# Kernel optimization log

Hardware: AMD Instinct MI355X
Metric: run time of the kernel (lower is better)

## Reference

```python
import jax, jax.numpy as jnp
import numpy as np

LOG_2PI = float(np.log(2.0 * np.pi))


def setup_inputs() -> dict:
    key = jax.random.key(0)
    k1, k2, k3 = jax.random.split(key, 3)
    B, C, D = 256, 1000, 256
    return {
        "x": jax.random.normal(k1, (B, D), dtype=jnp.float32),
        "metric_tensor": jax.random.normal(k2, (B, D, D), dtype=jnp.float32),
        "log_priors": jnp.zeros((C,), dtype=jnp.float32),
        "class_means": jax.random.normal(k3, (C, D), dtype=jnp.float32),
        "class_log_vars": jnp.zeros((C, D), dtype=jnp.float32),
    }


def reference(x, metric_tensor, log_priors, class_means, class_log_vars):
    D = x.shape[-1]
    # diff: [B, C, D]
    diff = x[:, None, :] - class_means[None, :, :]
    # Mahalanobis quadratic form per (batch, class): diff^T G diff
    maha = jnp.einsum("bcd,bde,bce->bc", diff, metric_tensor, diff)
    log_likelihood = -0.5 * (maha + jnp.sum(class_log_vars, axis=-1)[None, :] + D * LOG_2PI)
    log_posteriors = log_likelihood + log_priors[None, :]
    return jax.nn.log_softmax(log_posteriors, axis=-1)
```

## Files before the change

### kernel.cpp

```cpp
#include <hip/hip_runtime.h>

#define LOG2PI 1.83787706640934548356f

typedef __attribute__((ext_vector_type(4))) float f32x4;
typedef __attribute__((ext_vector_type(8))) short bf16x8;
typedef __attribute__((ext_vector_type(2))) unsigned int u32x2;

__device__ __forceinline__ unsigned short f2bf(float f) {
    union { float f; unsigned u; } v; v.f = f;
    unsigned r = v.u + 0x7fffu + ((v.u >> 16) & 1u);
    return (unsigned short)(r >> 16);
}
__device__ __forceinline__ bf16x8 pack8(f32x4 a, f32x4 b) {
    bf16x8 h;
    h[0]=(short)f2bf(a[0]); h[1]=(short)f2bf(a[1]); h[2]=(short)f2bf(a[2]); h[3]=(short)f2bf(a[3]);
    h[4]=(short)f2bf(b[0]); h[5]=(short)f2bf(b[1]); h[6]=(short)f2bf(b[2]); h[7]=(short)f2bf(b[3]);
    return h;
}

__global__ __launch_bounds__(256)
void k_prep(const float* __restrict__ clv, const float* __restrict__ lp,
            float* __restrict__ bias)
{
    const int w = threadIdx.x >> 6, lane = threadIdx.x & 63;
    const int c = blockIdx.x * 4 + w;
    if (c >= 1000) return;
    f32x4 v = *reinterpret_cast<const f32x4*>(clv + c * 256 + lane * 4);
    float s = v[0] + v[1] + v[2] + v[3];
    #pragma unroll
    for (int m = 1; m < 64; m <<= 1) s += __shfl_xor(s, m);
    if (lane == 0) bias[c] = lp[c] - 0.5f * (s + 256.0f * LOG2PI);
}

__global__ __launch_bounds__(256, 2)
void k_main(const float* __restrict__ x, const float* __restrict__ G,
            const float* __restrict__ means, float* __restrict__ out)
{
    __shared__ char dbuf[2][8192];
    __shared__ float maha[256];

    const int b     = blockIdx.x >> 2;
    const int cg    = blockIdx.x & 3;
    const int cbase = cg * 256;
    const int tid   = threadIdx.x;
    const int lane  = tid & 63;
    const int wn    = tid >> 6;
    const int lrow  = lane & 15;
    const int g     = lane >> 4;

    const float* Gb = G + (size_t)b * 65536;
    const float* xb = x + b * 256;

    maha[tid] = 0.f;

    bf16x8 greg[4][8];
    #pragma unroll
    for (int n = 0; n < 4; ++n) {
        const float* rowp = Gb + (size_t)(wn * 64 + n * 16 + lrow) * 256 + g * 8;
        #pragma unroll
        for (int ks = 0; ks < 8; ++ks) {
            f32x4 v0 = *reinterpret_cast<const f32x4*>(rowp + ks * 32);
            f32x4 v1 = *reinterpret_cast<const f32x4*>(rowp + ks * 32 + 4);
            greg[n][ks] = pack8(v0, v1);
        }
    }

    const int sr = tid & 15;
    const int s0 = tid >> 4;
    const int e0 = s0 * 8, e1 = e0 + 128;
    const f32x4 xa0 = *reinterpret_cast<const f32x4*>(xb + e0);
    const f32x4 xa1 = *reinterpret_cast<const f32x4*>(xb + e0 + 4);
    const f32x4 xb0 = *reinterpret_cast<const f32x4*>(xb + e1);
    const f32x4 xb1 = *reinterpret_cast<const f32x4*>(xb + e1 + 4);
    const int wbyte0 = (s0 * 16 + (sr ^ ((s0 & 3) << 1))) * 16;
    const int wbyte1 = wbyte0 + 4096;

    f32x4 r0a, r0b, r1a, r1b;
    auto load_chunk = [&](int c0) {
        int cc = cbase + c0 + sr; if (cc > 999) cc = 999;
        const float* mp = means + (size_t)cc * 256;
        r0a = *reinterpret_cast<const f32x4*>(mp + e0);
        r0b = *reinterpret_cast<const f32x4*>(mp + e0 + 4);
        r1a = *reinterpret_cast<const f32x4*>(mp + e1);
        r1b = *reinterpret_cast<const f32x4*>(mp + e1 + 4);
    };
    auto write_chunk = [&](int bufi) {
        *reinterpret_cast<bf16x8*>(dbuf[bufi] + wbyte0) = pack8(xa0 - r0a, xa1 - r0b);
        *reinterpret_cast<bf16x8*>(dbuf[bufi] + wbyte1) = pack8(xb0 - r1a, xb1 - r1b);
    };

    load_chunk(0);

    for (int t = 0; t < 16; ++t) {
        write_chunk(t & 1);
        __syncthreads();
        if (t < 15) load_chunk((t + 1) * 16);

        const char* buf = dbuf[t & 1];
        f32x4 acc[4];
        #pragma unroll
        for (int n = 0; n < 4; ++n) acc[n] = f32x4{0.f, 0.f, 0.f, 0.f};

        #pragma unroll
        for (int ks = 0; ks < 8; ++ks) {
            bf16x8 bfr = *reinterpret_cast<const bf16x8*>(
                buf + ((4 * ks + g) * 16 + (lrow ^ (g << 1))) * 16);
            #pragma unroll
            for (int n = 0; n < 4; ++n)
                acc[n] = __builtin_amdgcn_mfma_f32_16x16x32_bf16(greg[n][ks], bfr, acc[n], 0, 0, 0);
        }

        float p = 0.f;
        #pragma unroll
        for (int n = 0; n < 4; ++n) {
            const int d  = wn * 64 + n * 16 + g * 4;
            const int se = d >> 3;
            const int byte = (se * 16 + (lrow ^ ((se & 3) << 1))) * 16 + (d & 7) * 2;
            u32x2 dv = *reinterpret_cast<const u32x2*>(buf + byte);
            const float f0 = __uint_as_float(dv[0] << 16);
            const float f1 = __uint_as_float(dv[0] & 0xffff0000u);
            const float f2 = __uint_as_float(dv[1] << 16);
            const float f3 = __uint_as_float(dv[1] & 0xffff0000u);
            p += acc[n][0] * f0 + acc[n][1] * f1 + acc[n][2] * f2 + acc[n][3] * f3;
        }
        p += __shfl_xor(p, 16);
        p += __shfl_xor(p, 32);
        if (lane < 16) atomicAdd(&maha[t * 16 + lrow], p);
    }

    __syncthreads();
    const int c = cbase + tid;
    if (c < 1000) out[(size_t)b * 1000 + c] = maha[tid];
}

__global__ __launch_bounds__(256)
void k_soft(const float* __restrict__ bias, float* __restrict__ out)
{
    __shared__ float red[4];
    const int b = blockIdx.x, tid = threadIdx.x;
    const int lane = tid & 63, w = tid >> 6;
    float s[4];
    float mx = -3.4e38f;
    #pragma unroll
    for (int i = 0; i < 4; ++i) {
        const int c = tid + i * 256;
        if (c < 1000) {
            float v = -0.5f * out[(size_t)b * 1000 + c] + bias[c];
            s[i] = v; mx = fmaxf(mx, v);
        } else s[i] = -3.4e38f;
    }
    #pragma unroll
    for (int m = 1; m < 64; m <<= 1) mx = fmaxf(mx, __shfl_xor(mx, m));
    if (lane == 0) red[w] = mx;
    __syncthreads();
    const float bm = fmaxf(fmaxf(red[0], red[1]), fmaxf(red[2], red[3]));
    __syncthreads();
    float se = 0.f;
    #pragma unroll
    for (int i = 0; i < 4; ++i) {
        const int c = tid + i * 256;
        if (c < 1000) se += expf(s[i] - bm);
    }
    #pragma unroll
    for (int m = 1; m < 64; m <<= 1) se += __shfl_xor(se, m);
    if (lane == 0) red[w] = se;
    __syncthreads();
    const float lse = bm + logf(red[0] + red[1] + red[2] + red[3]);
    #pragma unroll
    for (int i = 0; i < 4; ++i) {
        const int c = tid + i * 256;
        if (c < 1000) out[(size_t)b * 1000 + c] = s[i] - lse;
    }
}

extern "C" void kernel_launch(void* const* d_in, const int* in_sizes, int n_in,
                              void* d_out, int out_size, void* d_ws, size_t ws_size,
                              hipStream_t stream)
{
    const float* x     = (const float*)d_in[0];
    const float* G     = (const float*)d_in[1];
    const float* lp    = (const float*)d_in[2];
    const float* means = (const float*)d_in[3];
    const float* clv   = (const float*)d_in[4];
    float* out  = (float*)d_out;
    float* bias = (float*)d_ws;

    k_prep<<<250, 256, 0, stream>>>(clv, lp, bias);
    k_main<<<1024, 256, 0, stream>>>(x, G, means, out);
    k_soft<<<256, 256, 0, stream>>>(bias, out);
}
```

Measured before the change: 182.7 us.

## Pre-convert metric tensor to bf16 in workspace before the main kernel

```diff
diff --git a/kernel.cpp b/kernel.cpp
--- a/kernel.cpp
+++ b/kernel.cpp
@@ -1,6 +1,7 @@
 #include <hip/hip_runtime.h>
 
 #define LOG2PI 1.83787706640934548356f
+#define NCONV 8192
 
 typedef __attribute__((ext_vector_type(4))) float f32x4;
 typedef __attribute__((ext_vector_type(8))) short bf16x8;
@@ -18,29 +19,53 @@
     return h;
 }
 
+__device__ __forceinline__ void prep_body(const float* __restrict__ clv,
+                                          const float* __restrict__ lp,
+                                          float* __restrict__ bias, int cblk)
+{
+    const int w = threadIdx.x >> 6, lane = threadIdx.x & 63;
+    const int c = cblk * 4 + w;
+    if (c >= 1000) return;
+    f32x4 v = *reinterpret_cast<const f32x4*>(clv + c * 256 + lane * 4);
+    float s = v[0] + v[1] + v[2] + v[3];
+    #pragma unroll
+    for (int m = 1; m < 64; m <<= 1) s += __shfl_xor(s, m);
+    if (lane == 0) bias[c] = lp[c] - 0.5f * (s + 256.0f * LOG2PI);
+}
+
+__global__ __launch_bounds__(256)
+void k_convprep(const float* __restrict__ G, unsigned short* __restrict__ Gt,
+                const float* __restrict__ clv, const float* __restrict__ lp,
+                float* __restrict__ bias)
+{
+    const int bid = blockIdx.x;
+    if (bid < NCONV) {
+        const size_t i = ((size_t)bid * 256 + threadIdx.x) * 8;
+        f32x4 a = *reinterpret_cast<const f32x4*>(G + i);
+        f32x4 b = *reinterpret_cast<const f32x4*>(G + i + 4);
+        *reinterpret_cast<bf16x8*>(Gt + i) = pack8(a, b);
+    } else {
+        prep_body(clv, lp, bias, bid - NCONV);
+    }
+}
+
 __global__ __launch_bounds__(256)
 void k_prep(const float* __restrict__ clv, const float* __restrict__ lp,
             float* __restrict__ bias)
 {
-    const int w = threadIdx.x >> 6, lane = threadIdx.x & 63;
-    const int c = blockIdx.x * 4 + w;
-    if (c >= 1000) return;
-    f32x4 v = *reinterpret_cast<const f32x4*>(clv + c * 256 + lane * 4);
-    float s = v[0] + v[1] + v[2] + v[3];
-    #pragma unroll
-    for (int m = 1; m < 64; m <<= 1) s += __shfl_xor(s, m);
-    if (lane == 0) bias[c] = lp[c] - 0.5f * (s + 256.0f * LOG2PI);
-}
-
+    prep_body(clv, lp, bias, blockIdx.x);
+}
+
+template <bool BF16G>
 __global__ __launch_bounds__(256, 2)
-void k_main(const float* __restrict__ x, const float* __restrict__ G,
+void k_main(const float* __restrict__ x, const void* __restrict__ Gsrc,
             const float* __restrict__ means, float* __restrict__ out)
 {
     __shared__ char dbuf[2][8192];
     __shared__ float maha[256];
 
-    const int b     = blockIdx.x >> 2;
-    const int cg    = blockIdx.x & 3;
+    const int b     = blockIdx.x & 255;
+    const int cg    = blockIdx.x >> 8;
     const int cbase = cg * 256;
     const int tid   = threadIdx.x;
     const int lane  = tid & 63;
@@ -48,20 +73,31 @@
     const int lrow  = lane & 15;
     const int g     = lane >> 4;
 
-    const float* Gb = G + (size_t)b * 65536;
     const float* xb = x + b * 256;
 
     maha[tid] = 0.f;
 
     bf16x8 greg[4][8];
-    #pragma unroll
-    for (int n = 0; n < 4; ++n) {
-        const float* rowp = Gb + (size_t)(wn * 64 + n * 16 + lrow) * 256 + g * 8;
-        #pragma unroll
-        for (int ks = 0; ks < 8; ++ks) {
-            f32x4 v0 = *reinterpret_cast<const f32x4*>(rowp + ks * 32);
-            f32x4 v1 = *reinterpret_cast<const f32x4*>(rowp + ks * 32 + 4);
-            greg[n][ks] = pack8(v0, v1);
+    if constexpr (BF16G) {
+        const unsigned short* Gb = (const unsigned short*)Gsrc + (size_t)b * 65536;
+        #pragma unroll
+        for (int n = 0; n < 4; ++n) {
+            const unsigned short* rowp = Gb + (size_t)(wn * 64 + n * 16 + lrow) * 256 + g * 8;
+            #pragma unroll
+            for (int ks = 0; ks < 8; ++ks)
+                greg[n][ks] = *reinterpret_cast<const bf16x8*>(rowp + ks * 32);
+        }
+    } else {
+        const float* Gb = (const float*)Gsrc + (size_t)b * 65536;
+        #pragma unroll
+        for (int n = 0; n < 4; ++n) {
+            const float* rowp = Gb + (size_t)(wn * 64 + n * 16 + lrow) * 256 + g * 8;
+            #pragma unroll
+            for (int ks = 0; ks < 8; ++ks) {
+                f32x4 v0 = *reinterpret_cast<const f32x4*>(rowp + ks * 32);
+                f32x4 v1 = *reinterpret_cast<const f32x4*>(rowp + ks * 32 + 4);
+                greg[n][ks] = pack8(v0, v1);
+            }
         }
     }
 
@@ -182,10 +218,19 @@
     const float* lp    = (const float*)d_in[2];
     const float* means = (const float*)d_in[3];
     const float* clv   = (const float*)d_in[4];
-    float* out  = (float*)d_out;
-    float* bias = (float*)d_ws;
-
-    k_prep<<<250, 256, 0, stream>>>(clv, lp, bias);
-    k_main<<<1024, 256, 0, stream>>>(x, G, means, out);
-    k_soft<<<256, 256, 0, stream>>>(bias, out);
-}
+    float* out = (float*)d_out;
+
+    const size_t need = (size_t)16777216 * 2 + 4096;
+    if (ws_size >= need) {
+        unsigned short* Gt = (unsigned short*)d_ws;
+        float* bias = (float*)((char*)d_ws + (size_t)16777216 * 2);
+        k_convprep<<<NCONV + 250, 256, 0, stream>>>(G, Gt, clv, lp, bias);
+        k_main<true><<<1024, 256, 0, stream>>>(x, (const void*)Gt, means, out);
+        k_soft<<<256, 256, 0, stream>>>(bias, out);
+    } else {
+        float* bias = (float*)d_ws;
+        k_prep<<<250, 256, 0, stream>>>(clv, lp, bias);
+        k_main<false><<<1024, 256, 0, stream>>>(x, (const void*)G, means, out);
+        k_soft<<<256, 256, 0, stream>>>(bias, out);
+    }
+}
```

Result: faster. 165.4 us (-9.5%).
